# Optimization experiments

Measured on AMD Instinct MI355X. Metric: run time of the kernel, lower is better.

The kernel has to match this reference:

```python
import jax, jax.numpy as jnp
import numpy as np

H = 20  # GRU hidden size (fixed in the module)


def gru_cell(x, h, Wih, Whh, bih, bhh):
    # PyTorch GRU cell math. x: (B, F), h: (B, H)
    gi = x @ Wih.T + bih  # (B, 3H)
    gh = h @ Whh.T + bhh  # (B, 3H)
    i_r, i_z, i_n = jnp.split(gi, 3, axis=-1)
    h_r, h_z, h_n = jnp.split(gh, 3, axis=-1)
    r = jax.nn.sigmoid(i_r + h_r)
    z = jax.nn.sigmoid(i_z + h_z)
    n = jnp.tanh(i_n + r * h_n)
    return (1.0 - z) * n + z * h


def setup_inputs() -> dict:
    key = jax.random.key(0)
    ks = jax.random.split(key, 16)
    B, S, R = 1024, 1024, 12
    F = R + 4 + 4 + 8 + 8  # 36 = input_record_width + embedding output_dim
    x = jax.random.normal(ks[0], (B, S, R), dtype=jnp.float32)
    onehots = jax.random.randint(ks[1], (B, S, 4), 0, 10, dtype=jnp.int64)
    s = 0.1
    inp = {
        'x': x, 'onehots': onehots,
        'emb0': jax.random.normal(ks[2], (10, 4), jnp.float32) * s,
        'emb1': jax.random.normal(ks[3], (20, 4), jnp.float32) * s,
        'emb2': jax.random.normal(ks[4], (50, 8), jnp.float32) * s,
        'emb3': jax.random.normal(ks[5], (100, 8), jnp.float32) * s,
        'Wih1': jax.random.normal(ks[6], (3 * H, F), jnp.float32) * s,
        'Whh1': jax.random.normal(ks[7], (3 * H, H), jnp.float32) * s,
        'bih1': jax.random.normal(ks[8], (3 * H,), jnp.float32) * s,
        'bhh1': jax.random.normal(ks[9], (3 * H,), jnp.float32) * s,
        'Wih2': jax.random.normal(ks[10], (3 * H, F), jnp.float32) * s,
        'Whh2': jax.random.normal(ks[11], (3 * H, H), jnp.float32) * s,
        'bih2': jax.random.normal(ks[12], (3 * H,), jnp.float32) * s,
        'bhh2': jax.random.normal(ks[13], (3 * H,), jnp.float32) * s,
        'Wfc': jax.random.normal(ks[14], (F, H), jnp.float32) * s,
        'bfc': jax.random.normal(ks[15], (F,), jnp.float32) * s,
    }
    return inp


def reference(x, onehots, emb0, emb1, emb2, emb3,
              Wih1, Whh1, bih1, bhh1, Wih2, Whh2, bih2, bhh2, Wfc, bfc):
    # Onehot embedding: lookup per categorical column, concat
    emb = jnp.concatenate([
        emb0[onehots[..., 0]], emb1[onehots[..., 1]],
        emb2[onehots[..., 2]], emb3[onehots[..., 3]],
    ], axis=-1)
    xin = jnp.concatenate([x, emb], axis=-1)  # (B, S, F)
    origin = xin
    B, S, F = xin.shape

    # Encoder GRU (gru1) over the sequence; keep only final hidden state
    h0 = jnp.zeros((B, H), xin.dtype)

    def enc_step(h, xt):
        return gru_cell(xt, h, Wih1, Whh1, bih1, bhh1), None

    h_last, _ = jax.lax.scan(enc_step, h0, jnp.swapaxes(xin, 0, 1))
    h = jnp.tanh(h_last)
    x0 = jnp.tanh(h @ Wfc.T + bfc)  # first decoded step

    def dec_step(carry, _):
        xprev, hprev = carry
        hnew = jnp.tanh(gru_cell(xprev, hprev, Wih2, Whh2, bih2, bhh2))
        xnew = jnp.tanh(hnew @ Wfc.T + bfc)
        return (xnew, hnew), xnew

    _, rest = jax.lax.scan(dec_step, (x0, h), None, length=S - 1)  # (S-1, B, F)
    xs = jnp.concatenate([x0[None], rest], axis=0)  # (S, B, F)
    xs = jnp.swapaxes(xs, 0, 1)[:, ::-1]  # (B, S, F), flipped along time
    return (origin, xs)
```

## Files before the change

kernel.cpp:

```cpp
#include <hip/hip_runtime.h>

#define BATCH 1024
#define SEQ   1024
#define FDIM  36
#define HID   20
#define G3    60
#define GIPAD 60
#define NROWS (BATCH*SEQ)
#define PROWS 16

typedef float v2f __attribute__((ext_vector_type(2)));

__device__ __forceinline__ float fast_sigmoid(float x){
    return __builtin_amdgcn_rcpf(1.0f + __expf(-x));
}
__device__ __forceinline__ float fast_tanh(float x){
    return fmaf(-2.0f, __builtin_amdgcn_rcpf(1.0f + __expf(2.0f*x)), 1.0f);
}

#define READLANE_F(v, u) __int_as_float(__builtin_amdgcn_readlane(__float_as_int(v), (u)))

template<bool WRITE_GI>
__global__ __launch_bounds__(256, 4)
void prep_kernel(const float* __restrict__ x,
                 const int* __restrict__ oh,
                 const float* __restrict__ e0, const float* __restrict__ e1,
                 const float* __restrict__ e2, const float* __restrict__ e3,
                 const float* __restrict__ Wih1g, const float* __restrict__ bih1g,
                 float* __restrict__ origin, float* __restrict__ gibuf)
{
    __shared__ __align__(16) float xsh[4][64];
    const int lane  = threadIdx.x & 63;
    const int wslot = threadIdx.x >> 6;
    const int w = blockIdx.x * 4 + wslot;
    const int r0 = w * PROWS;

    const int j = lane;
    const float* tbl; int ohc, eshift, sub;
    if (j < 16)      { tbl = e0; ohc = 0; eshift = 2; sub = j - 12; }
    else if (j < 20) { tbl = e1; ohc = 1; eshift = 2; sub = j - 16; }
    else if (j < 28) { tbl = e2; ohc = 2; eshift = 3; sub = j - 20; }
    else             { tbl = e3; ohc = 3; eshift = 3; sub = j - 28; }
    if (sub < 0) sub = 0;
    if (sub > 7) sub = 7;
    const bool from_x = (j < 12);
    const float* pa = from_x ? (x + j) : (tbl + sub);

    v2f w1p[FDIM/2]; float bi = 0.f;
    if (WRITE_GI) {
        const int k = lane < G3 ? lane : G3 - 1;
        #pragma unroll
        for (int q = 0; q < FDIM/2; q++) w1p[q] = ((const v2f*)(Wih1g + k * FDIM))[q];
        bi = bih1g[k];
    }

    int ohv[PROWS];
    #pragma unroll
    for (int s = 0; s < PROWS; s++) ohv[s] = oh[(r0 + s) * 4 + ohc];
    float valv[PROWS];
    #pragma unroll
    for (int s = 0; s < PROWS; s++) {
        int off = from_x ? ((r0 + s) * 12) : (ohv[s] << eshift);
        valv[s] = pa[off];
    }

    const float4* xp4 = (const float4*)xsh[wslot];
    #pragma unroll
    for (int s = 0; s < PROWS; s++) {
        const int row = r0 + s;
        if (lane < FDIM) origin[row * FDIM + lane] = valv[s];
        if (WRITE_GI) {
            xsh[wslot][lane] = valv[s];
            v2f a0 = {bi, 0.f}, a1 = {0.f, 0.f};
            #pragma unroll
            for (int q = 0; q < 9; q++) {
                float4 xv4 = xp4[q];
                v2f xlo = {xv4.x, xv4.y}, xhi = {xv4.z, xv4.w};
                a0 = __builtin_elementwise_fma(w1p[2*q],     xlo, a0);
                a1 = __builtin_elementwise_fma(w1p[2*q + 1], xhi, a1);
            }
            float g = (a0.x + a1.x) + (a0.y + a1.y);
            if (lane < G3) gibuf[row * GIPAD + lane] = g;
        }
    }
}

template<bool USE_GI>
__global__ __launch_bounds__(256, 1)
void gru_kernel(const float* __restrict__ xin,
                const float* __restrict__ gibuf,
                const float* __restrict__ Wih1g, const float* __restrict__ Whh1g,
                const float* __restrict__ bih1g, const float* __restrict__ bhh1g,
                const float* __restrict__ Wih2g, const float* __restrict__ Whh2g,
                const float* __restrict__ bih2g, const float* __restrict__ bhh2g,
                const float* __restrict__ Wfcg,  const float* __restrict__ bfcg,
                float* __restrict__ out2)
{
    __shared__ __align__(16) float xsh[4][64];
    const int lane  = threadIdx.x & 63;
    const int wslot = threadIdx.x >> 6;
    const int b = __builtin_amdgcn_readfirstlane(blockIdx.x * 4 + wslot);

    const int k  = lane < G3   ? lane : G3 - 1;
    const int kf = lane < FDIM ? lane : FDIM - 1;

    float whh1[HID], whh2[HID], wfc[HID];
    v2f wih2p[FDIM/2];
    #pragma unroll
    for (int u = 0; u < HID; u++) whh1[u] = Whh1g[k * HID + u];
    #pragma unroll
    for (int q = 0; q < FDIM/2; q++) wih2p[q] = ((const v2f*)(Wih2g + k * FDIM))[q];
    #pragma unroll
    for (int u = 0; u < HID; u++) whh2[u] = Whh2g[k * HID + u];
    #pragma unroll
    for (int u = 0; u < HID; u++) wfc[u] = Wfcg[kf * HID + u];
    const float bh1 = bhh1g[k];
    const float bi2 = bih2g[k], bh2 = bhh2g[k];
    const float bf  = bfcg[kf];

    float hs[HID];
    #pragma unroll
    for (int u = 0; u < HID; u++) hs[u] = 0.0f;
    float hv = 0.0f;

#define GATE_STEP(GIV, BH) do {                                              \
        float h0 = BH, h1 = 0.f, h2 = 0.f, h3 = 0.f;                         \
        _Pragma("unroll")                                                    \
        for (int uu = 0; uu < HID; uu += 4) {                                \
            h0 = fmaf(whh1[uu + 0], hs[uu + 0], h0);                         \
            h1 = fmaf(whh1[uu + 1], hs[uu + 1], h1);                         \
            h2 = fmaf(whh1[uu + 2], hs[uu + 2], h2);                         \
            h3 = fmaf(whh1[uu + 3], hs[uu + 3], h3);                         \
        }                                                                    \
        float gh = (h0 + h1) + (h2 + h3);                                    \
        float v   = (GIV) + gh;                                              \
        float vz  = __shfl(v,    (lane + 20) & 63);                          \
        float in_ = __shfl((GIV),(lane + 40) & 63);                          \
        float hn  = __shfl(gh,   (lane + 40) & 63);                          \
        float r = fast_sigmoid(v);                                           \
        float z = fast_sigmoid(vz);                                          \
        float n = fast_tanh(fmaf(r, hn, in_));                               \
        hv = n + z * (hv - n);                                               \
        _Pragma("unroll")                                                    \
        for (int uu = 0; uu < HID; uu++) hs[uu] = READLANE_F(hv, uu);        \
    } while (0)

    if (USE_GI) {
        const float* gb = gibuf + (size_t)b * SEQ * GIPAD + k;
        float gq[8];
        #pragma unroll
        for (int u = 0; u < 8; u++) gq[u] = gb[(size_t)u * GIPAD];
        for (int t = 0; t < SEQ; t += 8) {
            if (t + 8 < SEQ) {
                #pragma unroll
                for (int u = 0; u < 8; u++) {
                    float giv = gq[u];
                    gq[u] = gb[(size_t)(t + u + 8) * GIPAD];
                    GATE_STEP(giv, bh1);
                }
            } else {
                #pragma unroll
                for (int u = 0; u < 8; u++) {
                    GATE_STEP(gq[u], bh1);
                }
            }
        }
    } else {
        float wih1[FDIM]; float bi1;
        #pragma unroll
        for (int jj = 0; jj < FDIM; jj++) wih1[jj] = Wih1g[k * FDIM + jj];
        bi1 = bih1g[k];
        const float* xbase = xin + (size_t)b * SEQ * FDIM;
        float xa[FDIM];
        for (int t = 0; t < SEQ; t++) {
            const float* p = xbase + (size_t)t * FDIM;
            #pragma unroll
            for (int jj = 0; jj < FDIM; jj++) xa[jj] = p[jj];
            float g0 = bi1, g1 = 0.f, g2 = 0.f, g3 = 0.f;
            #pragma unroll
            for (int jj = 0; jj < FDIM; jj += 4) {
                g0 = fmaf(wih1[jj + 0], xa[jj + 0], g0);
                g1 = fmaf(wih1[jj + 1], xa[jj + 1], g1);
                g2 = fmaf(wih1[jj + 2], xa[jj + 2], g2);
                g3 = fmaf(wih1[jj + 3], xa[jj + 3], g3);
            }
            float giv = (g0 + g1) + (g2 + g3);
            GATE_STEP(giv, bh1);
        }
    }

    float hvd = fast_tanh(hv);
    #pragma unroll
    for (int u = 0; u < HID; u++) hs[u] = READLANE_F(hvd, u);

    float* orow = out2 + ((size_t)b * SEQ + (SEQ - 1)) * FDIM;

    float xv;
    {
        float a0 = bf, a1 = 0.f, a2 = 0.f, a3 = 0.f;
        #pragma unroll
        for (int u = 0; u < HID; u += 4) {
            a0 = fmaf(wfc[u + 0], hs[u + 0], a0);
            a1 = fmaf(wfc[u + 1], hs[u + 1], a1);
            a2 = fmaf(wfc[u + 2], hs[u + 2], a2);
            a3 = fmaf(wfc[u + 3], hs[u + 3], a3);
        }
        xv = fast_tanh((a0 + a1) + (a2 + a3));
    }
    if (lane < FDIM) orow[lane] = xv;
    xsh[wslot][lane] = xv;

    const v2f* xp = (const v2f*)xsh[wslot];
    for (int d = 1; d < SEQ; ++d) {
        orow -= FDIM;
        v2f xs2[FDIM/2];
        #pragma unroll
        for (int q = 0; q < FDIM/2; q++) xs2[q] = xp[q];
        float h0 = bh2, h1 = 0.f, h2 = 0.f, h3 = 0.f;
        #pragma unroll
        for (int u = 0; u < HID; u += 4) {
            h0 = fmaf(whh2[u + 0], hs[u + 0], h0);
            h1 = fmaf(whh2[u + 1], hs[u + 1], h1);
            h2 = fmaf(whh2[u + 2], hs[u + 2], h2);
            h3 = fmaf(whh2[u + 3], hs[u + 3], h3);
        }
        float gh = (h0 + h1) + (h2 + h3);
        v2f accA = {bi2, 0.f}, accB = {0.f, 0.f};
        #pragma unroll
        for (int q = 0; q < FDIM/2; q += 2) {
            accA = __builtin_elementwise_fma(wih2p[q],     xs2[q],     accA);
            accB = __builtin_elementwise_fma(wih2p[q + 1], xs2[q + 1], accB);
        }
        float gi = (accA.x + accB.x) + (accA.y + accB.y);
        float v   = gi + gh;
        float vz  = __shfl(v,  (lane + 20) & 63);
        float in_ = __shfl(gi, (lane + 40) & 63);
        float hn  = __shfl(gh, (lane + 40) & 63);
        float r = fast_sigmoid(v);
        float z = fast_sigmoid(vz);
        float n = fast_tanh(fmaf(r, hn, in_));
        float hraw = n + z * (hvd - n);
        hvd = fast_tanh(hraw);
        #pragma unroll
        for (int u = 0; u < HID; u++) hs[u] = READLANE_F(hvd, u);
        float a0 = bf, a1 = 0.f, a2 = 0.f, a3 = 0.f;
        #pragma unroll
        for (int u = 0; u < HID; u += 4) {
            a0 = fmaf(wfc[u + 0], hs[u + 0], a0);
            a1 = fmaf(wfc[u + 1], hs[u + 1], a1);
            a2 = fmaf(wfc[u + 2], hs[u + 2], a2);
            a3 = fmaf(wfc[u + 3], hs[u + 3], a3);
        }
        xv = fast_tanh((a0 + a1) + (a2 + a3));
        if (lane < FDIM) orow[lane] = xv;
        xsh[wslot][lane] = xv;
    }
}

extern "C" void kernel_launch(void* const* d_in, const int* in_sizes, int n_in,
                              void* d_out, int out_size, void* d_ws, size_t ws_size,
                              hipStream_t stream) {
    const float* x    = (const float*)d_in[0];
    const int*   oh   = (const int*)d_in[1];
    const float* e0   = (const float*)d_in[2];
    const float* e1   = (const float*)d_in[3];
    const float* e2   = (const float*)d_in[4];
    const float* e3   = (const float*)d_in[5];
    const float* Wih1 = (const float*)d_in[6];
    const float* Whh1 = (const float*)d_in[7];
    const float* bih1 = (const float*)d_in[8];
    const float* bhh1 = (const float*)d_in[9];
    const float* Wih2 = (const float*)d_in[10];
    const float* Whh2 = (const float*)d_in[11];
    const float* bih2 = (const float*)d_in[12];
    const float* bhh2 = (const float*)d_in[13];
    const float* Wfc  = (const float*)d_in[14];
    const float* bfc  = (const float*)d_in[15];

    float* out    = (float*)d_out;
    float* origin = out;
    float* out2   = out + (size_t)BATCH * SEQ * FDIM;
    float* gibuf  = (float*)d_ws;

    const size_t gi_bytes = (size_t)BATCH * SEQ * GIPAD * sizeof(float);
    const int prep_blocks = NROWS / (4 * PROWS);

    if (ws_size >= gi_bytes) {
        prep_kernel<true><<<prep_blocks, 256, 0, stream>>>(x, oh, e0, e1, e2, e3,
                                                           Wih1, bih1, origin, gibuf);
        gru_kernel<true><<<(BATCH * 64) / 256, 256, 0, stream>>>(origin, gibuf,
            Wih1, Whh1, bih1, bhh1, Wih2, Whh2, bih2, bhh2, Wfc, bfc, out2);
    } else {
        prep_kernel<false><<<prep_blocks, 256, 0, stream>>>(x, oh, e0, e1, e2, e3,
                                                            Wih1, bih1, origin, gibuf);
        gru_kernel<false><<<(BATCH * 64) / 256, 256, 0, stream>>>(origin, gibuf,
            Wih1, Whh1, bih1, bhh1, Wih2, Whh2, bih2, bhh2, Wfc, bfc, out2);
    }
}
```

Baseline: 1.020 ms.

## Compute all three GRU gates per lane to remove cross-lane shuffles in encoder

The encoder step now has each of 20 lanes compute the r, z and n hidden projections itself, using three register copies of the Whh1 rows. This replaces the three per-step __shfl exchanges on the serial critical path. To support this, the prep kernel writes the input-gate buffer interleaved as (unit, gate) triples so each lane reads three adjacent values, with a 4-deep prefetch queue. Per-lane FMA work triples and register pressure rises, in exchange for removing the shuffle latency from each recurrent step.

After: 1.139 ms. +11.7%, slower.

```diff
diff --git a/kernel.cpp b/kernel.cpp
--- a/kernel.cpp
+++ b/kernel.cpp
@@ -47,8 +47,9 @@
     const float* pa = from_x ? (x + j) : (tbl + sub);
 
     v2f w1p[FDIM/2]; float bi = 0.f;
+    const int k = lane < G3 ? lane : G3 - 1;
+    const int gidx = (k % HID) * 3 + (k / HID);
     if (WRITE_GI) {
-        const int k = lane < G3 ? lane : G3 - 1;
         #pragma unroll
         for (int q = 0; q < FDIM/2; q++) w1p[q] = ((const v2f*)(Wih1g + k * FDIM))[q];
         bi = bih1g[k];
@@ -80,7 +81,7 @@
                 a1 = __builtin_elementwise_fma(w1p[2*q + 1], xhi, a1);
             }
             float g = (a0.x + a1.x) + (a0.y + a1.y);
-            if (lane < G3) gibuf[row * GIPAD + lane] = g;
+            if (lane < G3) gibuf[row * GIPAD + gidx] = g;
         }
     }
 }
@@ -103,18 +104,25 @@
 
     const int k  = lane < G3   ? lane : G3 - 1;
     const int kf = lane < FDIM ? lane : FDIM - 1;
-
-    float whh1[HID], whh2[HID], wfc[HID];
+    const int u20 = lane < HID ? lane : HID - 1;
+
+    float whr[HID], whz[HID], whn[HID];
+    #pragma unroll
+    for (int u = 0; u < HID; u++) {
+        whr[u] = Whh1g[u20 * HID + u];
+        whz[u] = Whh1g[(HID + u20) * HID + u];
+        whn[u] = Whh1g[(2 * HID + u20) * HID + u];
+    }
+    const float bhr = bhh1g[u20], bhz = bhh1g[HID + u20], bhn = bhh1g[2 * HID + u20];
+
+    float whh2[HID], wfc[HID];
     v2f wih2p[FDIM/2];
     #pragma unroll
-    for (int u = 0; u < HID; u++) whh1[u] = Whh1g[k * HID + u];
-    #pragma unroll
     for (int q = 0; q < FDIM/2; q++) wih2p[q] = ((const v2f*)(Wih2g + k * FDIM))[q];
     #pragma unroll
     for (int u = 0; u < HID; u++) whh2[u] = Whh2g[k * HID + u];
     #pragma unroll
     for (int u = 0; u < HID; u++) wfc[u] = Wfcg[kf * HID + u];
-    const float bh1 = bhh1g[k];
     const float bi2 = bih2g[k], bh2 = bhh2g[k];
     const float bf  = bfcg[kf];
 
@@ -123,69 +131,77 @@
     for (int u = 0; u < HID; u++) hs[u] = 0.0f;
     float hv = 0.0f;
 
-#define GATE_STEP(GIV, BH) do {                                              \
-        float h0 = BH, h1 = 0.f, h2 = 0.f, h3 = 0.f;                         \
+#define ENC_GATES(GIR, GIZ, GIN) do {                                        \
+        float a0 = bhr, a1 = 0.f, a2 = 0.f, a3 = 0.f;                        \
+        float c0 = bhz, c1 = 0.f, c2 = 0.f, c3 = 0.f;                        \
+        float d0 = bhn, d1 = 0.f, d2 = 0.f, d3 = 0.f;                        \
         _Pragma("unroll")                                                    \
         for (int uu = 0; uu < HID; uu += 4) {                                \
-            h0 = fmaf(whh1[uu + 0], hs[uu + 0], h0);                         \
-            h1 = fmaf(whh1[uu + 1], hs[uu + 1], h1);                         \
-            h2 = fmaf(whh1[uu + 2], hs[uu + 2], h2);                         \
-            h3 = fmaf(whh1[uu + 3], hs[uu + 3], h3);                         \
+            a0 = fmaf(whr[uu + 0], hs[uu + 0], a0);                          \
+            a1 = fmaf(whr[uu + 1], hs[uu + 1], a1);                          \
+            a2 = fmaf(whr[uu + 2], hs[uu + 2], a2);                          \
+            a3 = fmaf(whr[uu + 3], hs[uu + 3], a3);                          \
+            c0 = fmaf(whz[uu + 0], hs[uu + 0], c0);                          \
+            c1 = fmaf(whz[uu + 1], hs[uu + 1], c1);                          \
+            c2 = fmaf(whz[uu + 2], hs[uu + 2], c2);                          \
+            c3 = fmaf(whz[uu + 3], hs[uu + 3], c3);                          \
+            d0 = fmaf(whn[uu + 0], hs[uu + 0], d0);                          \
+            d1 = fmaf(whn[uu + 1], hs[uu + 1], d1);                          \
+            d2 = fmaf(whn[uu + 2], hs[uu + 2], d2);                          \
+            d3 = fmaf(whn[uu + 3], hs[uu + 3], d3);                          \
         }                                                                    \
-        float gh = (h0 + h1) + (h2 + h3);                                    \
-        float v   = (GIV) + gh;                                              \
-        float vz  = __shfl(v,    (lane + 20) & 63);                          \
-        float in_ = __shfl((GIV),(lane + 40) & 63);                          \
-        float hn  = __shfl(gh,   (lane + 40) & 63);                          \
-        float r = fast_sigmoid(v);                                           \
-        float z = fast_sigmoid(vz);                                          \
-        float n = fast_tanh(fmaf(r, hn, in_));                               \
+        float ghr = (a0 + a1) + (a2 + a3);                                   \
+        float ghz = (c0 + c1) + (c2 + c3);                                   \
+        float ghn = (d0 + d1) + (d2 + d3);                                   \
+        float r = fast_sigmoid((GIR) + ghr);                                 \
+        float z = fast_sigmoid((GIZ) + ghz);                                 \
+        float n = fast_tanh(fmaf(r, ghn, (GIN)));                            \
         hv = n + z * (hv - n);                                               \
         _Pragma("unroll")                                                    \
         for (int uu = 0; uu < HID; uu++) hs[uu] = READLANE_F(hv, uu);        \
     } while (0)
 
     if (USE_GI) {
-        const float* gb = gibuf + (size_t)b * SEQ * GIPAD + k;
-        float gq[8];
-        #pragma unroll
-        for (int u = 0; u < 8; u++) gq[u] = gb[(size_t)u * GIPAD];
-        for (int t = 0; t < SEQ; t += 8) {
-            if (t + 8 < SEQ) {
-                #pragma unroll
-                for (int u = 0; u < 8; u++) {
-                    float giv = gq[u];
-                    gq[u] = gb[(size_t)(t + u + 8) * GIPAD];
-                    GATE_STEP(giv, bh1);
-                }
-            } else {
-                #pragma unroll
-                for (int u = 0; u < 8; u++) {
-                    GATE_STEP(gq[u], bh1);
-                }
+        const float* gp = gibuf + (size_t)b * SEQ * GIPAD + u20 * 3;
+        float q0[4], q1[4], q2[4];
+        #pragma unroll
+        for (int s = 0; s < 4; s++) {
+            const float* pp = gp + s * GIPAD;
+            q0[s] = pp[0]; q1[s] = pp[1]; q2[s] = pp[2];
+        }
+        for (int t = 0; t < SEQ; t += 4) {
+            #pragma unroll
+            for (int ss = 0; ss < 4; ss++) {
+                float gir = q0[ss], giz = q1[ss], gin = q2[ss];
+                int tn = t + ss + 4; tn = tn < SEQ ? tn : SEQ - 1;
+                const float* pp = gp + (size_t)tn * GIPAD;
+                q0[ss] = pp[0]; q1[ss] = pp[1]; q2[ss] = pp[2];
+                ENC_GATES(gir, giz, gin);
             }
         }
     } else {
-        float wih1[FDIM]; float bi1;
-        #pragma unroll
-        for (int jj = 0; jj < FDIM; jj++) wih1[jj] = Wih1g[k * FDIM + jj];
-        bi1 = bih1g[k];
+        float wir[FDIM], wiz[FDIM], win[FDIM];
+        #pragma unroll
+        for (int jj = 0; jj < FDIM; jj++) {
+            wir[jj] = Wih1g[u20 * FDIM + jj];
+            wiz[jj] = Wih1g[(HID + u20) * FDIM + jj];
+            win[jj] = Wih1g[(2 * HID + u20) * FDIM + jj];
+        }
+        const float bir = bih1g[u20], biz = bih1g[HID + u20], bin = bih1g[2 * HID + u20];
         const float* xbase = xin + (size_t)b * SEQ * FDIM;
-        float xa[FDIM];
         for (int t = 0; t < SEQ; t++) {
             const float* p = xbase + (size_t)t * FDIM;
+            float xa[FDIM];
             #pragma unroll
             for (int jj = 0; jj < FDIM; jj++) xa[jj] = p[jj];
-            float g0 = bi1, g1 = 0.f, g2 = 0.f, g3 = 0.f;
+            float gr = bir, gz = biz, gn = bin;
             #pragma unroll
-            for (int jj = 0; jj < FDIM; jj += 4) {
-                g0 = fmaf(wih1[jj + 0], xa[jj + 0], g0);
-                g1 = fmaf(wih1[jj + 1], xa[jj + 1], g1);
-                g2 = fmaf(wih1[jj + 2], xa[jj + 2], g2);
-                g3 = fmaf(wih1[jj + 3], xa[jj + 3], g3);
+            for (int jj = 0; jj < FDIM; jj++) {
+                gr = fmaf(wir[jj], xa[jj], gr);
+                gz = fmaf(wiz[jj], xa[jj], gz);
+                gn = fmaf(win[jj], xa[jj], gn);
             }
-            float giv = (g0 + g1) + (g2 + g3);
-            GATE_STEP(giv, bh1);
+            ENC_GATES(gr, gz, gn);
         }
     }
 
```
